# Kernel tuning notes

Hardware: AMD Instinct MI355X
Metric: run time of the kernel (lower is better)

Reference implementation:

```python
import jax, jax.numpy as jnp
import numpy as np
from jax import lax

TOPK = 2


def setup_inputs() -> dict:
    key = jax.random.key(0)
    k1, k2, k3, k4 = jax.random.split(key, 4)
    B, T, D, E = 4, 2048, 1024, 8
    x = jax.random.normal(k1, (B, T, D), dtype=jnp.float32)
    gate_w = jax.random.normal(k2, (E, D), dtype=jnp.float32) * 0.02
    w_fc = jax.random.normal(k3, (E, 4 * D, D), dtype=jnp.float32) * 0.02
    w_proj = jax.random.normal(k4, (E, D, 4 * D), dtype=jnp.float32) * 0.02
    return {"x": x, "gate_w": gate_w, "w_fc": w_fc, "w_proj": w_proj}


def reference(x, gate_w, w_fc, w_proj):
    B, T, D = x.shape
    E = gate_w.shape[0]
    N = B * T
    xf = x.reshape(N, D)

    # gating
    gate_logits = xf @ gate_w.T                      # [N, E]
    gate_probs = jax.nn.softmax(gate_logits, axis=-1)
    routing_weights, expert_indices = lax.top_k(gate_probs, TOPK)  # [N, K]
    routing_weights = routing_weights / routing_weights.sum(axis=-1, keepdims=True)

    # combine weights per (token, expert); top-k indices are distinct per token
    hot = jax.nn.one_hot(expert_indices, E, dtype=xf.dtype)        # [N, K, E]
    comb = jnp.einsum('nke,nk->ne', hot, routing_weights)          # [N, E]
    tok_sel = hot.sum(axis=1)                                      # [N, E] in {0,1}
    expert_freq = tok_sel.mean(axis=0)                             # [E]

    # per-expert MLP (relu^2), accumulated over experts via scan
    def step(acc, xs):
        w1, w2, ce = xs                      # [4D,D], [D,4D], [N]
        h = jnp.square(jax.nn.relu(xf @ w1.T))   # [N, 4D]
        y = h @ w2.T                             # [N, D]
        return acc + ce[:, None] * y, None

    out, _ = lax.scan(step, jnp.zeros_like(xf), (w_fc, w_proj, comb.T))
    out = out.reshape(B, T, D)

    balance_loss = (gate_probs.mean(axis=0) * lax.stop_gradient(expert_freq)).sum() * E
    return out, balance_loss
```

## Files before the change

### kernel.cpp

```cpp
#include <hip/hip_runtime.h>
#include <hip/hip_bf16.h>

#define NTOK 8192
#define DDIM 1024
#define HDIM 4096
#define NEXP 8
#define NPAIR (NTOK * 2)
#define NMTILE 136
#define NPADROW (NPAIR + NEXP * 128)

typedef __attribute__((ext_vector_type(8))) short short8;
typedef __attribute__((ext_vector_type(4))) float floatx4;

__device__ __forceinline__ unsigned short f2bf(float f) {
  unsigned u = __float_as_uint(f);
  u += 0x7fffu + ((u >> 16) & 1u);
  return (unsigned short)(u >> 16);
}

__device__ __forceinline__ void async_copy16(const void* g, void* l) {
  __builtin_amdgcn_global_load_lds(
      (const __attribute__((address_space(1))) unsigned int*)g,
      (__attribute__((address_space(3))) unsigned int*)l, 16, 0, 0);
}

__global__ void cast_kernel(const float* __restrict__ src,
                            unsigned short* __restrict__ dst, int n4) {
  int i = blockIdx.x * 256 + threadIdx.x;
  if (i >= n4) return;
  const float4 v = ((const float4*)src)[i];
  ushort4 o;
  o.x = f2bf(v.x); o.y = f2bf(v.y); o.z = f2bf(v.z); o.w = f2bf(v.w);
  ((ushort4*)dst)[i] = o;
}

__global__ __launch_bounds__(256) void gating_kernel(
    const float* __restrict__ x, const float* __restrict__ gw,
    int* __restrict__ selE, float* __restrict__ selW,
    int* __restrict__ cnt, float* __restrict__ psum) {
  __shared__ float gws[NEXP * DDIM];
  __shared__ float pblk[4][NEXP];
  __shared__ int cblk[NEXP];
  const int t = threadIdx.x;
  for (int i = t; i < NEXP * DDIM; i += 256) gws[i] = gw[i];
  if (t < NEXP) cblk[t] = 0;
  __syncthreads();
  const int wv = t >> 6, lane = t & 63;
  const int tok = blockIdx.x * 4 + wv;
  double acc[NEXP];
#pragma unroll
  for (int e = 0; e < NEXP; e++) acc[e] = 0.0;
  const float* xr = x + (size_t)tok * DDIM;
  for (int i = lane; i < DDIM; i += 64) {
    double xv = (double)xr[i];
#pragma unroll
    for (int e = 0; e < NEXP; e++) acc[e] += xv * (double)gws[e * DDIM + i];
  }
#pragma unroll
  for (int e = 0; e < NEXP; e++)
    for (int off = 32; off > 0; off >>= 1) acc[e] += __shfl_xor(acc[e], off, 64);
  if (lane == 0) {
    double mx = acc[0];
    for (int e = 1; e < NEXP; e++) mx = acc[e] > mx ? acc[e] : mx;
    double p[NEXP], s = 0.0;
    for (int e = 0; e < NEXP; e++) { p[e] = exp(acc[e] - mx); s += p[e]; }
    int e1 = 0; double b1 = p[0];
    for (int e = 1; e < NEXP; e++) if (p[e] > b1) { b1 = p[e]; e1 = e; }
    int e2 = -1; double b2 = -1.0;
    for (int e = 0; e < NEXP; e++) if (e != e1 && p[e] > b2) { b2 = p[e]; e2 = e; }
    double rs = b1 + b2;
    selE[tok * 2 + 0] = e1; selE[tok * 2 + 1] = e2;
    selW[tok * 2 + 0] = (float)(b1 / rs); selW[tok * 2 + 1] = (float)(b2 / rs);
    atomicAdd(&cblk[e1], 1); atomicAdd(&cblk[e2], 1);
    for (int e = 0; e < NEXP; e++) pblk[wv][e] = (float)(p[e] / s);
  }
  __syncthreads();
  if (t < NEXP) {
    float sp = pblk[0][t] + pblk[1][t] + pblk[2][t] + pblk[3][t];
    atomicAdd(&psum[t], sp);
    if (cblk[t]) atomicAdd(&cnt[t], cblk[t]);
  }
}

__global__ void finalize_kernel(const int* __restrict__ cnt,
                                const float* __restrict__ psum,
                                int* __restrict__ abase, int* __restrict__ fill,
                                int* __restrict__ tile2exp,
                                float* __restrict__ loss_out) {
  for (int t = 0; t < NMTILE; t++) tile2exp[t] = -1;
  int b = 0;
  for (int e = 0; e < NEXP; e++) {
    abase[e] = b;
    fill[e] = b;
    int nt = (cnt[e] + 127) >> 7;
    for (int j = 0; j < nt; j++) tile2exp[(b >> 7) + j] = e;
    b += nt << 7;
  }
  abase[NEXP] = b;
  double L = 0.0;
  for (int e = 0; e < NEXP; e++) L += (double)psum[e] * (double)cnt[e];
  *loss_out = (float)(L * (double)NEXP / ((double)NTOK * (double)NTOK));
}

__global__ void scatter_kernel(const int* __restrict__ selE,
                               const float* __restrict__ selW,
                               int* __restrict__ fill, int* __restrict__ pairtok,
                               float* __restrict__ pairw, int* __restrict__ invmap) {
  int n = blockIdx.x * 256 + threadIdx.x;
  if (n >= NTOK) return;
  for (int k = 0; k < 2; k++) {
    int e = selE[n * 2 + k];
    int pos = atomicAdd(&fill[e], 1);
    pairtok[pos] = n;
    pairw[pos] = selW[n * 2 + k];
    invmap[n * 2 + k] = pos;
  }
}

__global__ __launch_bounds__(256) void combine_kernel(
    const float* __restrict__ ybuf, const int* __restrict__ invmap,
    float* __restrict__ out) {
  const int tok = blockIdx.x;
  const int c = threadIdx.x;
  const int p1 = invmap[tok * 2 + 0];
  const int p2 = invmap[tok * 2 + 1];
  const float4 a = ((const float4*)(ybuf + (size_t)p1 * DDIM))[c];
  const float4 b = ((const float4*)(ybuf + (size_t)p2 * DDIM))[c];
  float4 o;
  o.x = a.x + b.x; o.y = a.y + b.y; o.z = a.z + b.z; o.w = a.w + b.w;
  ((float4*)(out + (size_t)tok * DDIM))[c] = o;
}

template <int KD, int ND, int MODE>
__global__ __launch_bounds__(256) void moe_gemm(
    const unsigned short* __restrict__ A, const unsigned short* __restrict__ B,
    const int* __restrict__ abase, const int* __restrict__ cnt,
    const int* __restrict__ tile2exp, const int* __restrict__ pairtok,
    const float* __restrict__ pairw, unsigned short* __restrict__ hbuf,
    float* __restrict__ ybuf) {
  const int mtile = blockIdx.y;
  const int e = tile2exp[mtile];
  if (e < 0) return;
  const int m0 = abase[e];
  const int cntE = cnt[e];
  const int mloc = mtile * 128 - m0;
  const int ntile = blockIdx.x;

  __shared__ unsigned short ldsA[512 * 8];
  __shared__ unsigned short ldsB[512 * 8];

  const int t = threadIdx.x, w = t >> 6, lane = t & 63;

  const unsigned short* gA[2];
  const unsigned short* gB[2];
  unsigned short* dstA[2];
  unsigned short* dstB[2];
#pragma unroll
  for (int i = 0; i < 2; i++) {
    const int c = w * 128 + i * 64 + lane;
    const int row = c >> 2;
    const int q = (c & 3) ^ (row & 3) ^ ((row >> 2) & 3);
    dstA[i] = ldsA + (w * 128 + i * 64) * 8;
    dstB[i] = ldsB + (w * 128 + i * 64) * 8;
    int ar = mloc + row;
    if (ar > cntE - 1) ar = cntE - 1;
    size_t arow;
    if (MODE == 0) arow = (size_t)pairtok[m0 + ar];
    else           arow = (size_t)(m0 + ar);
    gA[i] = A + arow * (size_t)KD + q * 8;
    gB[i] = B + ((size_t)e * ND + (ntile * 128 + row)) * (size_t)KD + q * 8;
  }

  const int wm = (w & 1) * 64, wn = (w >> 1) * 64;
  const int sw = (lane >> 4) ^ (lane & 3) ^ ((lane >> 2) & 3);
  const short8* aptr[4];
  const short8* bptr[4];
#pragma unroll
  for (int i = 0; i < 4; i++) {
    aptr[i] = (const short8*)ldsA + (wm + i * 16 + (lane & 15)) * 4 + sw;
    bptr[i] = (const short8*)ldsB + (wn + i * 16 + (lane & 15)) * 4 + sw;
  }

  floatx4 acc[4][4] = {};

  for (int kt = 0; kt < KD / 32; kt++) {
#pragma unroll
    for (int i = 0; i < 2; i++) {
      async_copy16(gA[i] + kt * 32, dstA[i]);
      async_copy16(gB[i] + kt * 32, dstB[i]);
    }
    __syncthreads();
    short8 a[4], b[4];
#pragma unroll
    for (int i = 0; i < 4; i++) { a[i] = *aptr[i]; b[i] = *bptr[i]; }
#pragma unroll
    for (int im = 0; im < 4; im++)
#pragma unroll
      for (int in = 0; in < 4; in++)
        acc[im][in] = __builtin_amdgcn_mfma_f32_16x16x32_bf16(a[im], b[in], acc[im][in], 0, 0, 0);
    __syncthreads();
  }

  const int Mv = cntE - mloc;
#pragma unroll
  for (int im = 0; im < 4; im++) {
#pragma unroll
    for (int r = 0; r < 4; r++) {
      const int rl = wm + im * 16 + (lane >> 4) * 4 + r;
      if (rl < Mv) {
        const int pr = m0 + mloc + rl;
        if (MODE == 0) {
#pragma unroll
          for (int in = 0; in < 4; in++) {
            float v = acc[im][in][r];
            v = v > 0.f ? v * v : 0.f;
            const int col = ntile * 128 + wn + in * 16 + (lane & 15);
            hbuf[(size_t)pr * HDIM + col] = f2bf(v);
          }
        } else {
          const float wgt = pairw[pr];
          float* yrow = ybuf + (size_t)pr * DDIM;
#pragma unroll
          for (int in = 0; in < 4; in++) {
            const int col = ntile * 128 + wn + in * 16 + (lane & 15);
            yrow[col] = wgt * acc[im][in][r];
          }
        }
      }
    }
  }
}

extern "C" void kernel_launch(void* const* d_in, const int* in_sizes, int n_in,
                              void* d_out, int out_size, void* d_ws, size_t ws_size,
                              hipStream_t stream) {
  const float* x   = (const float*)d_in[0];
  const float* gw  = (const float*)d_in[1];
  const float* wfc = (const float*)d_in[2];
  const float* wpj = (const float*)d_in[3];
  float* out = (float*)d_out;

  char* ws = (char*)d_ws;
  size_t off = 0;
  auto alloc = [&](size_t bytes) -> void* {
    void* p = ws + off;
    off += (bytes + 255) & ~(size_t)255;
    return p;
  };
  unsigned short* xb   = (unsigned short*)alloc((size_t)NTOK * DDIM * 2);
  unsigned short* wfcb = (unsigned short*)alloc((size_t)NEXP * HDIM * DDIM * 2);
  unsigned short* wpjb = (unsigned short*)alloc((size_t)NEXP * DDIM * HDIM * 2);
  unsigned short* hbuf = (unsigned short*)alloc((size_t)NPADROW * HDIM * 2);
  float* ybuf          = (float*)alloc((size_t)NPADROW * DDIM * 4);
  int*   pairtok = (int*)alloc(NPADROW * 4);
  float* pairw   = (float*)alloc(NPADROW * 4);
  int*   invmap  = (int*)alloc(NPAIR * 4);
  int*   selE    = (int*)alloc(NTOK * 2 * 4);
  float* selW    = (float*)alloc(NTOK * 2 * 4);
  int*   ctr     = (int*)alloc(1024);
  int* cnt = ctr; int* fill = ctr + 8; int* abase = ctr + 16;
  float* psum = (float*)(ctr + 28);
  int* tile2exp = ctr + 40;

  hipMemsetAsync(ctr, 0, 1024, stream);

  cast_kernel<<<(NTOK * DDIM / 4 + 255) / 256, 256, 0, stream>>>(x, xb, NTOK * DDIM / 4);
  cast_kernel<<<(NEXP * HDIM * DDIM / 4 + 255) / 256, 256, 0, stream>>>(wfc, wfcb, NEXP * HDIM * DDIM / 4);
  cast_kernel<<<(NEXP * DDIM * HDIM / 4 + 255) / 256, 256, 0, stream>>>(wpj, wpjb, NEXP * DDIM * HDIM / 4);

  gating_kernel<<<NTOK / 4, 256, 0, stream>>>(x, gw, selE, selW, cnt, psum);
  finalize_kernel<<<1, 1, 0, stream>>>(cnt, psum, abase, fill, tile2exp,
                                       out + (size_t)NTOK * DDIM);
  scatter_kernel<<<NTOK / 256, 256, 0, stream>>>(selE, selW, fill, pairtok, pairw, invmap);

  moe_gemm<DDIM, HDIM, 0><<<dim3(HDIM / 128, NMTILE), 256, 0, stream>>>(
      xb, wfcb, abase, cnt, tile2exp, pairtok, pairw, hbuf, nullptr);
  moe_gemm<HDIM, DDIM, 1><<<dim3(DDIM / 128, NMTILE), 256, 0, stream>>>(
      hbuf, wpjb, abase, cnt, tile2exp, pairtok, pairw, nullptr, ybuf);

  combine_kernel<<<NTOK, 256, 0, stream>>>(ybuf, invmap, out);
}
```

Baseline: 886.7 us.

## Double-buffer LDS tiles in MoE GEMM and remap workgroups per XCD

Splits the LDS staging buffers into two halves so that the async global-to-LDS copies for the next K slice are issued while MFMAs consume the current slice. This hides load latency and drops one barrier per iteration. It also remaps the linear workgroup id so that consecutive tiles go to the same XCD, which should improve L2 reuse of the shared A/B rows. The cost is doubled LDS usage per block, which may lower occupancy.

```diff
diff --git a/kernel.cpp b/kernel.cpp
--- a/kernel.cpp
+++ b/kernel.cpp
@@ -138,30 +138,38 @@
     const int* __restrict__ tile2exp, const int* __restrict__ pairtok,
     const float* __restrict__ pairw, unsigned short* __restrict__ hbuf,
     float* __restrict__ ybuf) {
-  const int mtile = blockIdx.y;
+  constexpr int NT = ND / 128;
+  constexpr int KT = KD / 32;
+
+  const int nwg = NT * NMTILE;
+  const int lid = blockIdx.y * NT + blockIdx.x;
+  const int q8 = nwg >> 3, r8 = nwg & 7;
+  const int xcd = lid & 7, sub = lid >> 3;
+  const int cbase = (xcd < r8) ? xcd * (q8 + 1) : r8 * (q8 + 1) + (xcd - r8) * q8;
+  const int nlid = cbase + sub;
+  const int mtile = nlid / NT;
+  const int ntile = nlid - mtile * NT;
+
   const int e = tile2exp[mtile];
   if (e < 0) return;
   const int m0 = abase[e];
   const int cntE = cnt[e];
   const int mloc = mtile * 128 - m0;
-  const int ntile = blockIdx.x;
-
-  __shared__ unsigned short ldsA[512 * 8];
-  __shared__ unsigned short ldsB[512 * 8];
+
+  __shared__ unsigned short ldsA[2][4096];
+  __shared__ unsigned short ldsB[2][4096];
 
   const int t = threadIdx.x, w = t >> 6, lane = t & 63;
 
   const unsigned short* gA[2];
   const unsigned short* gB[2];
-  unsigned short* dstA[2];
-  unsigned short* dstB[2];
+  int soff[2];
 #pragma unroll
   for (int i = 0; i < 2; i++) {
     const int c = w * 128 + i * 64 + lane;
     const int row = c >> 2;
     const int q = (c & 3) ^ (row & 3) ^ ((row >> 2) & 3);
-    dstA[i] = ldsA + (w * 128 + i * 64) * 8;
-    dstB[i] = ldsB + (w * 128 + i * 64) * 8;
+    soff[i] = (w * 128 + i * 64) * 8;
     int ar = mloc + row;
     if (ar > cntE - 1) ar = cntE - 1;
     size_t arow;
@@ -173,26 +181,38 @@
 
   const int wm = (w & 1) * 64, wn = (w >> 1) * 64;
   const int sw = (lane >> 4) ^ (lane & 3) ^ ((lane >> 2) & 3);
-  const short8* aptr[4];
-  const short8* bptr[4];
+  int aoff[4], boff[4];
 #pragma unroll
   for (int i = 0; i < 4; i++) {
-    aptr[i] = (const short8*)ldsA + (wm + i * 16 + (lane & 15)) * 4 + sw;
-    bptr[i] = (const short8*)ldsB + (wn + i * 16 + (lane & 15)) * 4 + sw;
+    aoff[i] = (wm + i * 16 + (lane & 15)) * 4 + sw;
+    boff[i] = (wn + i * 16 + (lane & 15)) * 4 + sw;
   }
 
   floatx4 acc[4][4] = {};
 
-  for (int kt = 0; kt < KD / 32; kt++) {
-#pragma unroll
-    for (int i = 0; i < 2; i++) {
-      async_copy16(gA[i] + kt * 32, dstA[i]);
-      async_copy16(gB[i] + kt * 32, dstB[i]);
+#pragma unroll
+  for (int i = 0; i < 2; i++) {
+    async_copy16(gA[i], &ldsA[0][soff[i]]);
+    async_copy16(gB[i], &ldsB[0][soff[i]]);
+  }
+  __syncthreads();
+
+#pragma unroll 2
+  for (int kt = 0; kt < KT; kt++) {
+    const int cur = kt & 1;
+    if (kt + 1 < KT) {
+#pragma unroll
+      for (int i = 0; i < 2; i++) {
+        async_copy16(gA[i] + (kt + 1) * 32, &ldsA[cur ^ 1][soff[i]]);
+        async_copy16(gB[i] + (kt + 1) * 32, &ldsB[cur ^ 1][soff[i]]);
+      }
     }
-    __syncthreads();
     short8 a[4], b[4];
 #pragma unroll
-    for (int i = 0; i < 4; i++) { a[i] = *aptr[i]; b[i] = *bptr[i]; }
+    for (int i = 0; i < 4; i++) {
+      a[i] = ((const short8*)ldsA[cur])[aoff[i]];
+      b[i] = ((const short8*)ldsB[cur])[boff[i]];
+    }
 #pragma unroll
     for (int im = 0; im < 4; im++)
 #pragma unroll
```

Measured after the change: 889.3 us. About the same (+0.3%).
